# Performance work log

Measured on AMD Instinct MI355X. Metric: run time of the kernel, lower is better.

Reference implementation:

```python
import jax, jax.numpy as jnp
import numpy as np
import math

NUM_BANDS = 8
BINS = 512
CROPSIZE = 1024
BATCH = 4


def _dwconv(x, w, b):
    # depthwise Conv1d, kernel=3, padding=1, groups=C. x: [B,C,W], w: [C,1,3], b: [C]
    y = jax.lax.conv_general_dilated(x, w, window_strides=(1,), padding=((1, 1),),
                                     feature_group_count=x.shape[1])
    return y + b[None, :, None]


def setup_inputs() -> dict:
    key = jax.random.key(0)
    ks = jax.random.split(key, 20)
    s = 0.02
    lin = lambda k: jax.random.normal(k, (BINS, BINS), jnp.float32) * s
    cw = lambda k: jax.random.normal(k, (BINS, 1, 3), jnp.float32) * s
    vec = lambda k: jax.random.normal(k, (BINS,), jnp.float32) * s
    return {
        "x": jax.random.normal(ks[0], (BATCH, CROPSIZE, BINS), jnp.float32),
        "q_w": lin(ks[1]), "q_b": vec(ks[2]), "q_cw": cw(ks[3]), "q_cb": vec(ks[4]),
        "k_w": lin(ks[5]), "k_b": vec(ks[6]), "k_cw": cw(ks[7]), "k_cb": vec(ks[8]),
        "v_w": lin(ks[9]), "v_b": vec(ks[10]), "v_cw": cw(ks[11]), "v_cb": vec(ks[12]),
        "o_w": lin(ks[13]), "o_b": vec(ks[14]),
        "er": jax.random.normal(ks[15], (BINS // NUM_BANDS, CROPSIZE), jnp.float32),
    }


def reference(x, q_w, q_b, q_cw, q_cb, k_w, k_b, k_cw, k_cb,
              v_w, v_b, v_cw, v_cb, o_w, o_b, er):
    b, w, c = x.shape
    h = NUM_BANDS

    def proj(lw, lb, cwt, cbt):
        y = x @ lw.T + lb                                   # [b,w,c] linear
        y = _dwconv(y.transpose(0, 2, 1), cwt, cbt)         # [b,c,w] depthwise conv
        return y.transpose(0, 2, 1).reshape(b, w, h, -1)    # [b,w,h,d]

    q = proj(q_w, q_b, q_cw, q_cb).transpose(0, 2, 1, 3)    # [b,h,w,d]
    k = proj(k_w, k_b, k_cw, k_cb).transpose(0, 2, 3, 1)    # [b,h,d,w]
    v = proj(v_w, v_b, v_cw, v_cb).transpose(0, 2, 1, 3)    # [b,h,w,d]

    # relative position bias via pad/transpose/slice skew
    qe = jnp.einsum('bhwd,dc->bhwc', q, er)                 # [b,h,w,cropsize]
    p = jnp.pad(qe, ((0, 0), (0, 0), (0, 0), (1, 0)))       # [b,h,w,cs+1]
    p = p.transpose(0, 1, 3, 2)[:, :, 1:, :]                # [b,h,cs,w] == [b,h,w,w]

    qk = (q @ k + p) / math.sqrt(c)
    a = jax.nn.softmax(qk, axis=-1)
    out = (a @ v).transpose(0, 2, 1, 3).reshape(b, w, c)    # [b,w,c]
    return out @ o_w.T + o_b
```

## Files before the change

### kernel.cpp

```cpp
#include <hip/hip_runtime.h>
#include <hip/hip_bf16.h>
#include <math.h>


#define CROP 1024
#define NB 512
#define NH 8
#define HD 64
#define NBATCH 4
#define MTOT 4096
#define NBH 32
#define JSPLIT 4
#define ROWS_TOT 32768

typedef __attribute__((ext_vector_type(8))) short bf8;
typedef __attribute__((ext_vector_type(4))) short s4;
typedef __attribute__((ext_vector_type(4))) float f4;
typedef __attribute__((ext_vector_type(8))) _Float16 h8;

__device__ __forceinline__ short f2bf(float f) {
  __hip_bfloat16 h = __float2bfloat16(f);
  short s;
  __builtin_memcpy(&s, &h, 2);
  return s;
}
__device__ __forceinline__ float bf2f(short s) {
  union { unsigned u; float f; } v; v.u = ((unsigned)(unsigned short)s) << 16;
  return v.f;
}
__device__ __forceinline__ f4 mfma16(bf8 a, bf8 b, f4 c) {
  return __builtin_amdgcn_mfma_f32_16x16x32_bf16(a, b, c, 0, 0, 0);
}
__device__ __forceinline__ float fast_exp2(float x) {
#if __has_builtin(__builtin_amdgcn_exp2f)
  return __builtin_amdgcn_exp2f(x);
#else
  float r;
  asm("v_exp_f32 %0, %1" : "=v"(r) : "v"(x));
  return r;
#endif
}

__device__ __forceinline__ void stage16(const short* g, short* ldsbase, int lane) {
#if __has_builtin(__builtin_amdgcn_global_load_lds)
  __builtin_amdgcn_global_load_lds(
      (const __attribute__((address_space(1))) void*)g,
      (__attribute__((address_space(3))) void*)ldsbase, 16, 0, 0);
#else
  *(bf8*)(ldsbase + lane * 8) = *(const bf8*)g;
#endif
}

#define ISC 0.044194173824159216f
#define QSCALE 0.06376743237228177f

__global__ __launch_bounds__(256) void prep_kernel(
    const float* __restrict__ x,
    const float* __restrict__ w0, const float* __restrict__ w1,
    const float* __restrict__ w2, const float* __restrict__ w3,
    const float* __restrict__ er,
    short* __restrict__ xb, short* __restrict__ wb, short* __restrict__ erT)
{
  const int blk = blockIdx.x;
  const int t = threadIdx.x;
  if (blk < 1024) {
    int i = (blk * 256 + t) * 8;
    f4 a = *(const f4*)(x + i);
    f4 b = *(const f4*)(x + i + 4);
    bf8 o;
#pragma unroll
    for (int j = 0; j < 4; ++j) { o[j] = f2bf(a[j]); o[4 + j] = f2bf(b[j]); }
    *(bf8*)(xb + i) = o;
  } else if (blk < 1536) {
    int p = (blk - 1024) >> 7;
    const float* s = (p == 0) ? w0 : (p == 1) ? w1 : (p == 2) ? w2 : w3;
    int i = (((blk - 1024) & 127) * 256 + t) * 8;
    f4 a = *(const f4*)(s + i);
    f4 b = *(const f4*)(s + i + 4);
    bf8 o;
#pragma unroll
    for (int j = 0; j < 4; ++j) { o[j] = f2bf(a[j]); o[4 + j] = f2bf(b[j]); }
    *(bf8*)(wb + (size_t)p * NB * NB + i) = o;
  } else {
    int idx = (blk - 1536) * 256 + t;
    int w = idx >> 6, d = idx & 63;
    erT[idx] = f2bf(er[d * CROP + w]);
  }
}

__device__ __forceinline__ void gemm128_loop(
    const short* __restrict__ A, const short* __restrict__ Bm,
    short* As, short* Bs, int rowA0, int rowB0, f4 (&acc)[4][4], int t)
{
  const int lane = t & 63, wave = t >> 6;
  const int wr = wave >> 1, wc = wave & 1;
  const int l15 = lane & 15, l4 = lane >> 4;
  const int crow = lane >> 3;
  const int csub = lane & 7;
  const int kb = (csub * 16) ^ (crow << 4);

  for (int k0 = 0; k0 < NB; k0 += 64) {
    __syncthreads();
#pragma unroll
    for (int i = 0; i < 4; ++i) {
      const int c = wave * 4 + i;
      stage16(A + (size_t)(rowA0 + c * 8 + crow) * NB + k0 + (kb >> 1),
              As + c * 512, lane);
      stage16(Bm + (size_t)(rowB0 + c * 8 + crow) * NB + k0 + (kb >> 1),
              Bs + c * 512, lane);
    }
    __syncthreads();
#pragma unroll
    for (int ks = 0; ks < 2; ++ks) {
      bf8 af[4], bg[4];
#pragma unroll
      for (int mt = 0; mt < 4; ++mt) {
        const int row = wr * 64 + mt * 16 + l15;
        const int byt = (ks * 64 + l4 * 16) ^ ((row & 7) << 4);
        af[mt] = *(const bf8*)&As[row * 64 + (byt >> 1)];
      }
#pragma unroll
      for (int nt = 0; nt < 4; ++nt) {
        const int row = wc * 64 + nt * 16 + l15;
        const int byt = (ks * 64 + l4 * 16) ^ ((row & 7) << 4);
        bg[nt] = *(const bf8*)&Bs[row * 64 + (byt >> 1)];
      }
#pragma unroll
      for (int mt = 0; mt < 4; ++mt)
#pragma unroll
        for (int nt = 0; nt < 4; ++nt)
          acc[mt][nt] = mfma16(af[mt], bg[nt], acc[mt][nt]);
    }
  }
}

__global__ __launch_bounds__(256) void proj_gemm3(
    const short* __restrict__ Xb, const short* __restrict__ Wb,
    const float* __restrict__ B0, const float* __restrict__ B1, const float* __restrict__ B2,
    short* __restrict__ O0, short* __restrict__ O1, short* __restrict__ O2)
{
  __shared__ short As[128 * 64];
  __shared__ short Bs[128 * 64];
  f4 acc[4][4];
#pragma unroll
  for (int i = 0; i < 4; ++i)
#pragma unroll
    for (int j = 0; j < 4; ++j) acc[i][j] = (f4){0.f, 0.f, 0.f, 0.f};

  const int bm = blockIdx.x, bn = blockIdx.y;
  gemm128_loop(Xb, Wb, As, Bs, bm * 128, bn * 128, acc, threadIdx.x);

  const int p = bn >> 2;
  const float* Bb = (p == 0) ? B0 : (p == 1) ? B1 : B2;
  short* Out = (p == 0) ? O0 : (p == 1) ? O1 : O2;
  const int ncol0 = (bn & 3) * 128;

  const int t = threadIdx.x;
  const int lane = t & 63, wave = t >> 6;
  const int wr = wave >> 1, wc = wave & 1;
  const int l15 = lane & 15, l4 = lane >> 4;
#pragma unroll
  for (int mt = 0; mt < 4; ++mt)
#pragma unroll
    for (int nt = 0; nt < 4; ++nt) {
      const int col = ncol0 + wc * 64 + nt * 16 + l15;
      const float bias = Bb[col];
#pragma unroll
      for (int r = 0; r < 4; ++r) {
        const int row = bm * 128 + wr * 64 + mt * 16 + l4 * 4 + r;
        Out[(size_t)row * NB + col] = f2bf(acc[mt][nt][r] + bias);
      }
    }
}

__global__ __launch_bounds__(256) void dwconv_all(
    const short* __restrict__ q0p, const short* __restrict__ k0p,
    const short* __restrict__ v0p,
    const float* __restrict__ qcw, const float* __restrict__ qcb,
    const float* __restrict__ kcw, const float* __restrict__ kcb,
    const float* __restrict__ vcw, const float* __restrict__ vcb,
    short* __restrict__ qb, short* __restrict__ kb, short* __restrict__ vb)
{
  const int blk = blockIdx.x;
  const int t = threadIdx.x;

  if (blk < 2048) {
    const int p = blk >> 10;
    const short* src = p ? k0p : q0p;
    const float* cw = p ? kcw : qcw;
    const float* cb = p ? kcb : qcb;
    short* dst = p ? kb : qb;
    const float scale = p ? 1.0f : QSCALE;

    const int idx = ((blk & 1023) * 256 + t) * 8;
    const int c = idx & (NB - 1);
    const int m = idx >> 9;
    const int w = m & (CROP - 1);
    const int b = m >> 10;

    const bf8 z = (bf8){0, 0, 0, 0, 0, 0, 0, 0};
    bf8 mid = *(const bf8*)(src + idx);
    bf8 lo = (w > 0) ? *(const bf8*)(src + idx - NB) : z;
    bf8 hi = (w < CROP - 1) ? *(const bf8*)(src + idx + NB) : z;

    f4 cwv[6];
#pragma unroll
    for (int i = 0; i < 6; ++i) cwv[i] = *(const f4*)(cw + c * 3 + i * 4);
    f4 cb0 = *(const f4*)(cb + c);
    f4 cb1 = *(const f4*)(cb + c + 4);

    bf8 o;
#pragma unroll
    for (int j = 0; j < 8; ++j) {
      float k0w = cwv[(3 * j) >> 2][(3 * j) & 3];
      float k1w = cwv[(3 * j + 1) >> 2][(3 * j + 1) & 3];
      float k2w = cwv[(3 * j + 2) >> 2][(3 * j + 2) & 3];
      float bias = (j < 4) ? cb0[j] : cb1[j - 4];
      float acc = bias + k0w * bf2f(lo[j]) + k1w * bf2f(mid[j]) + k2w * bf2f(hi[j]);
      o[j] = f2bf(acc * scale);
    }
    const int h = c >> 6, d0 = c & 63;
    *(bf8*)(dst + ((size_t)(b * NH + h) * CROP + w) * HD + d0) = o;
  } else {
    __shared__ short S[66][72];
    const int blk2 = blk - 2048;
    const int w0 = (blk2 & 15) * 64, c0 = ((blk2 >> 4) & 7) * 64, b = blk2 >> 7;

#pragma unroll
    for (int i = 0; i < 3; ++i) {
      int r = i * 32 + (t >> 3);
      if (r < 66) {
        int w = w0 - 1 + r;
        int cg = (t & 7) * 8;
        bf8 val = (bf8){0, 0, 0, 0, 0, 0, 0, 0};
        if (w >= 0 && w < CROP)
          val = *(const bf8*)(v0p + ((size_t)b * CROP + w) * NB + c0 + cg);
        *(bf8*)&S[r][cg] = val;
      }
    }
    __syncthreads();

    const int c = t & 63, wv = t >> 6;
    const float k0w = vcw[(c0 + c) * 3 + 0];
    const float k1w = vcw[(c0 + c) * 3 + 1];
    const float k2w = vcw[(c0 + c) * 3 + 2];
    const float bias = vcb[c0 + c];

    float xa = bf2f(S[wv * 16][c]);
    float xb2 = bf2f(S[wv * 16 + 1][c]);
    short res[16];
#pragma unroll
    for (int ww = 0; ww < 16; ++ww) {
      float xc = bf2f(S[wv * 16 + ww + 2][c]);
      res[ww] = f2bf(bias + k0w * xa + k1w * xb2 + k2w * xc);
      xa = xb2; xb2 = xc;
    }
    short* dstbase = vb + ((size_t)(b * NB) + c0 + c) * CROP + w0
                     + (wv >> 1) * 32 + (wv & 1) * 4;
#pragma unroll
    for (int pidx = 0; pidx < 4; ++pidx)
      *(s4*)(dstbase + pidx * 8) = *(s4*)&res[pidx * 4];
  }
}

__global__ __launch_bounds__(512) void attn_part(
    const short* __restrict__ Qb, const short* __restrict__ Kb,
    const short* __restrict__ Vb, const short* __restrict__ ErT,
    _Float16* __restrict__ Op, float* __restrict__ lbuf)
{
  __shared__ short Ks[64][72];
  __shared__ short Qs[64][72];
  __shared__ short Vs[64][72];

  const int qt = blockIdx.x, bh = blockIdx.y, s = blockIdx.z;
  const int t = threadIdx.x;
  const int lane = t & 63, wave = t >> 6;
  const int l15 = lane & 15, l4 = lane >> 4;
  const int wq = qt * 128 + wave * 16;

  bf8 qa[2], ea[2];
  {
    const short* qrow = Qb + ((size_t)bh * CROP + wq + l15) * HD + l4 * 8;
    qa[0] = *(const bf8*)(qrow);
    qa[1] = *(const bf8*)(qrow + 32);
    const short* erow = ErT + (size_t)(wq + l15) * HD + l4 * 8;
    ea[0] = *(const bf8*)(erow);
    ea[1] = *(const bf8*)(erow + 32);
  }

  float lsum = 0.f;
  f4 oacc[4];
#pragma unroll
  for (int nt = 0; nt < 4; ++nt) oacc[nt] = (f4){0.f, 0.f, 0.f, 0.f};

  const int sr2 = t >> 3, sc2 = (t & 7) * 8;
  const short* ksrc = Kb + ((size_t)bh * CROP + sr2) * HD + sc2;
  const short* qsrc = Qb + ((size_t)bh * CROP + sr2) * HD + sc2;
  const short* vsrc = Vb + ((size_t)bh * HD + sr2) * CROP + sc2;

  const int jbase = s * (CROP / JSPLIT);
  const int JLEN = CROP / JSPLIT;

  bf8 rk = *(const bf8*)(ksrc + jbase * HD);
  bf8 rq = *(const bf8*)(qsrc + jbase * HD);
  bf8 rv = *(const bf8*)(vsrc + jbase);

  for (int jj = 0; jj < JLEN; jj += 64) {
    __syncthreads();
    *(bf8*)&Ks[sr2][sc2] = rk;
    *(bf8*)&Qs[sr2][sc2] = rq;
    *(bf8*)&Vs[sr2][sc2] = rv;
    __syncthreads();

    const int jn = jj + 64;
    if (jn < JLEN) {
      rk = *(const bf8*)(ksrc + (jbase + jn) * HD);
      rq = *(const bf8*)(qsrc + (jbase + jn) * HD);
      rv = *(const bf8*)(vsrc + jbase + jn);
    }

    f4 sacc[4];
#pragma unroll
    for (int nt = 0; nt < 4; ++nt) sacc[nt] = (f4){0.f, 0.f, 0.f, 0.f};
    __builtin_amdgcn_s_setprio(1);
#pragma unroll
    for (int ks = 0; ks < 2; ++ks) {
#pragma unroll
      for (int nt = 0; nt < 4; ++nt) {
        bf8 kf = *(bf8*)&Ks[nt * 16 + l15][ks * 32 + l4 * 8];
        sacc[nt] = mfma16(kf, qa[ks], sacc[nt]);
        bf8 qf = *(bf8*)&Qs[nt * 16 + l15][ks * 32 + l4 * 8];
        sacc[nt] = mfma16(qf, ea[ks], sacc[nt]);
      }
    }
    __builtin_amdgcn_s_setprio(0);

    bf8 pf0, pf1;
#pragma unroll
    for (int nt = 0; nt < 4; ++nt) {
      float e0 = fast_exp2(sacc[nt][0]);
      float e1 = fast_exp2(sacc[nt][1]);
      float e2 = fast_exp2(sacc[nt][2]);
      float e3 = fast_exp2(sacc[nt][3]);
      lsum += (e0 + e1) + (e2 + e3);
      if (nt < 2) {
        pf0[nt * 4 + 0] = f2bf(e0); pf0[nt * 4 + 1] = f2bf(e1);
        pf0[nt * 4 + 2] = f2bf(e2); pf0[nt * 4 + 3] = f2bf(e3);
      } else {
        pf1[(nt - 2) * 4 + 0] = f2bf(e0); pf1[(nt - 2) * 4 + 1] = f2bf(e1);
        pf1[(nt - 2) * 4 + 2] = f2bf(e2); pf1[(nt - 2) * 4 + 3] = f2bf(e3);
      }
    }

    __builtin_amdgcn_s_setprio(1);
#pragma unroll
    for (int ks = 0; ks < 2; ++ks) {
      bf8 pf = ks ? pf1 : pf0;
#pragma unroll
      for (int nt = 0; nt < 4; ++nt) {
        bf8 vf = *(bf8*)&Vs[nt * 16 + l15][ks * 32 + l4 * 8];
        oacc[nt] = mfma16(pf, vf, oacc[nt]);
      }
    }
    __builtin_amdgcn_s_setprio(0);
  }

  lsum += __shfl_xor(lsum, 16);
  lsum += __shfl_xor(lsum, 32);

#pragma unroll
  for (int r = 0; r < 4; ++r) {
    const int row = wq + l4 * 4 + r;
    const size_t ridx = (size_t)(s * NBH + bh) * CROP + row;
#pragma unroll
    for (int nt = 0; nt < 4; ++nt)
      Op[ridx * HD + nt * 16 + l15] = (_Float16)oacc[nt][r];
  }
  if (lane < 16)
    lbuf[(size_t)(s * NBH + bh) * CROP + wq + l15] = lsum;
}

__global__ __launch_bounds__(256) void attn_combine(
    const _Float16* __restrict__ Op, const float* __restrict__ lbuf,
    short* __restrict__ Ao)
{
  const int t = threadIdx.x;
  const int idx = blockIdx.x * 32 + (t >> 3);
  const int dth = (t & 7) * 8;
  float l = 0.f;
#pragma unroll
  for (int s = 0; s < JSPLIT; ++s) l += lbuf[(size_t)s * ROWS_TOT + idx];
  float inv = 1.f / l;
  float o[8] = {0, 0, 0, 0, 0, 0, 0, 0};
#pragma unroll
  for (int s = 0; s < JSPLIT; ++s) {
    h8 v = *(const h8*)(Op + ((size_t)s * ROWS_TOT + idx) * HD + dth);
#pragma unroll
    for (int j = 0; j < 8; ++j) o[j] += (float)v[j];
  }
  const int bh = idx >> 10, row = idx & (CROP - 1);
  const int b = bh >> 3, h = bh & 7;
  short* dst = Ao + ((size_t)(b * CROP + row)) * NB + h * HD + dth;
  bf8 ov;
#pragma unroll
  for (int j = 0; j < 8; ++j) ov[j] = f2bf(o[j] * inv);
  *(bf8*)dst = ov;
}

__global__ __launch_bounds__(256) void out_gemm2(
    const short* __restrict__ A, const short* __restrict__ Wt,
    const float* __restrict__ Bb, float* __restrict__ Out)
{
  __shared__ short As[64][72];
  __shared__ short Bs[64][72];
  const int t = threadIdx.x;
  const int lane = t & 63, wave = t >> 6;
  const int wr = wave >> 1, wc = wave & 1;
  const int l15 = lane & 15, l4 = lane >> 4;
  const int bm = blockIdx.x, bn = blockIdx.y;

  f4 acc[2][2];
#pragma unroll
  for (int i = 0; i < 2; ++i)
#pragma unroll
    for (int j = 0; j < 2; ++j) acc[i][j] = (f4){0.f, 0.f, 0.f, 0.f};

  const int sr = t >> 2, sc = (t & 3) * 16;
  const short* arow = A + (size_t)(bm * 64 + sr) * NB + sc;
  const short* wrow = Wt + (size_t)(bn * 64 + sr) * NB + sc;

  for (int k0 = 0; k0 < NB; k0 += 64) {
    bf8 a0 = *(const bf8*)(arow + k0);
    bf8 a1 = *(const bf8*)(arow + k0 + 8);
    bf8 b0 = *(const bf8*)(wrow + k0);
    bf8 b1 = *(const bf8*)(wrow + k0 + 8);
    __syncthreads();
    *(bf8*)&As[sr][sc] = a0;
    *(bf8*)&As[sr][sc + 8] = a1;
    *(bf8*)&Bs[sr][sc] = b0;
    *(bf8*)&Bs[sr][sc + 8] = b1;
    __syncthreads();
#pragma unroll
    for (int ks = 0; ks < 2; ++ks) {
      bf8 af[2], bg[2];
#pragma unroll
      for (int mt = 0; mt < 2; ++mt)
        af[mt] = *(bf8*)&As[wr * 32 + mt * 16 + l15][ks * 32 + l4 * 8];
#pragma unroll
      for (int nt = 0; nt < 2; ++nt)
        bg[nt] = *(bf8*)&Bs[wc * 32 + nt * 16 + l15][ks * 32 + l4 * 8];
#pragma unroll
      for (int mt = 0; mt < 2; ++mt)
#pragma unroll
        for (int nt = 0; nt < 2; ++nt)
          acc[mt][nt] = mfma16(af[mt], bg[nt], acc[mt][nt]);
    }
  }
#pragma unroll
  for (int mt = 0; mt < 2; ++mt)
#pragma unroll
    for (int nt = 0; nt < 2; ++nt)
#pragma unroll
      for (int r = 0; r < 4; ++r) {
        int row = bm * 64 + wr * 32 + mt * 16 + l4 * 4 + r;
        int col = bn * 64 + wc * 32 + nt * 16 + l15;
        Out[(size_t)row * NB + col] = acc[mt][nt][r] + Bb[col];
      }
}

extern "C" void kernel_launch(void* const* d_in, const int* in_sizes, int n_in,
                              void* d_out, int out_size, void* d_ws, size_t ws_size,
                              hipStream_t stream) {
  (void)in_sizes; (void)n_in; (void)out_size; (void)ws_size;
  const float* x    = (const float*)d_in[0];
  const float* q_w  = (const float*)d_in[1];
  const float* q_b  = (const float*)d_in[2];
  const float* q_cw = (const float*)d_in[3];
  const float* q_cb = (const float*)d_in[4];
  const float* k_w  = (const float*)d_in[5];
  const float* k_b  = (const float*)d_in[6];
  const float* k_cw = (const float*)d_in[7];
  const float* k_cb = (const float*)d_in[8];
  const float* v_w  = (const float*)d_in[9];
  const float* v_b  = (const float*)d_in[10];
  const float* v_cw = (const float*)d_in[11];
  const float* v_cb = (const float*)d_in[12];
  const float* o_w  = (const float*)d_in[13];
  const float* o_b  = (const float*)d_in[14];
  const float* er   = (const float*)d_in[15];
  float* out = (float*)d_out;

  char* ws = (char*)d_ws;
  const size_t MB = 1u << 20;
  short* q0  = (short*)(ws + 0 * MB);
  short* k0  = (short*)(ws + 4 * MB);
  short* v0  = (short*)(ws + 8 * MB);
  short* qb2 = (short*)(ws + 12 * MB);
  short* kb2 = (short*)(ws + 16 * MB);
  short* vb2 = (short*)(ws + 20 * MB);
  short* ao  = (short*)(ws + 24 * MB);
  short* erT = (short*)(ws + 28 * MB);
  short* xb  = (short*)(ws + 29 * MB);
  short* wb  = (short*)(ws + 33 * MB);
  _Float16* Op = (_Float16*)(ws + 36 * MB);
  float* lbuf  = (float*)(ws + 52 * MB);

  prep_kernel<<<dim3(1792), dim3(256), 0, stream>>>(
      x, q_w, k_w, v_w, o_w, er, xb, wb, erT);
  proj_gemm3<<<dim3(32, 12), dim3(256), 0, stream>>>(
      xb, wb, q_b, k_b, v_b, q0, k0, v0);
  dwconv_all<<<dim3(2560), dim3(256), 0, stream>>>(
      q0, k0, v0, q_cw, q_cb, k_cw, k_cb, v_cw, v_cb, qb2, kb2, vb2);
  attn_part<<<dim3(8, NBH, JSPLIT), dim3(512), 0, stream>>>(
      qb2, kb2, vb2, erT, Op, lbuf);
  attn_combine<<<dim3(1024), dim3(256), 0, stream>>>(Op, lbuf, ao);
  out_gemm2<<<dim3(64, 8), dim3(256), 0, stream>>>(
      ao, wb + 3 * NB * NB, o_b, out);
}
```

Before: 69.06 us.

## Process two query subtiles per wave in attention with 256-thread blocks

```diff
diff --git a/kernel.cpp b/kernel.cpp
--- a/kernel.cpp
+++ b/kernel.cpp
@@ -263,7 +263,7 @@
   }
 }
 
-__global__ __launch_bounds__(512) void attn_part(
+__global__ __launch_bounds__(256) void attn_part(
     const short* __restrict__ Qb, const short* __restrict__ Kb,
     const short* __restrict__ Vb, const short* __restrict__ ErT,
     _Float16* __restrict__ Op, float* __restrict__ lbuf)
@@ -276,22 +276,25 @@
   const int t = threadIdx.x;
   const int lane = t & 63, wave = t >> 6;
   const int l15 = lane & 15, l4 = lane >> 4;
-  const int wq = qt * 128 + wave * 16;
-
-  bf8 qa[2], ea[2];
-  {
-    const short* qrow = Qb + ((size_t)bh * CROP + wq + l15) * HD + l4 * 8;
-    qa[0] = *(const bf8*)(qrow);
-    qa[1] = *(const bf8*)(qrow + 32);
-    const short* erow = ErT + (size_t)(wq + l15) * HD + l4 * 8;
-    ea[0] = *(const bf8*)(erow);
-    ea[1] = *(const bf8*)(erow + 32);
-  }
-
-  float lsum = 0.f;
-  f4 oacc[4];
-#pragma unroll
-  for (int nt = 0; nt < 4; ++nt) oacc[nt] = (f4){0.f, 0.f, 0.f, 0.f};
+  const int wq = qt * 128 + wave * 32;
+
+  bf8 qa[2][2], ea[2][2];
+#pragma unroll
+  for (int ih = 0; ih < 2; ++ih) {
+    const short* qrow = Qb + ((size_t)bh * CROP + wq + ih * 16 + l15) * HD + l4 * 8;
+    qa[ih][0] = *(const bf8*)(qrow);
+    qa[ih][1] = *(const bf8*)(qrow + 32);
+    const short* erow = ErT + (size_t)(wq + ih * 16 + l15) * HD + l4 * 8;
+    ea[ih][0] = *(const bf8*)(erow);
+    ea[ih][1] = *(const bf8*)(erow + 32);
+  }
+
+  float lsum[2] = {0.f, 0.f};
+  f4 oacc[2][4];
+#pragma unroll
+  for (int ih = 0; ih < 2; ++ih)
+#pragma unroll
+    for (int nt = 0; nt < 4; ++nt) oacc[ih][nt] = (f4){0.f, 0.f, 0.f, 0.f};
 
   const int sr2 = t >> 3, sc2 = (t & 7) * 8;
   const short* ksrc = Kb + ((size_t)bh * CROP + sr2) * HD + sc2;
@@ -301,83 +304,102 @@
   const int jbase = s * (CROP / JSPLIT);
   const int JLEN = CROP / JSPLIT;
 
-  bf8 rk = *(const bf8*)(ksrc + jbase * HD);
-  bf8 rq = *(const bf8*)(qsrc + jbase * HD);
-  bf8 rv = *(const bf8*)(vsrc + jbase);
+  bf8 rk0 = *(const bf8*)(ksrc + jbase * HD);
+  bf8 rk1 = *(const bf8*)(ksrc + (jbase + 32) * HD);
+  bf8 rq0 = *(const bf8*)(qsrc + jbase * HD);
+  bf8 rq1 = *(const bf8*)(qsrc + (jbase + 32) * HD);
+  bf8 rv0 = *(const bf8*)(vsrc + jbase);
+  bf8 rv1 = *(const bf8*)(vsrc + 32 * CROP + jbase);
 
   for (int jj = 0; jj < JLEN; jj += 64) {
     __syncthreads();
-    *(bf8*)&Ks[sr2][sc2] = rk;
-    *(bf8*)&Qs[sr2][sc2] = rq;
-    *(bf8*)&Vs[sr2][sc2] = rv;
+    *(bf8*)&Ks[sr2][sc2] = rk0;
+    *(bf8*)&Ks[32 + sr2][sc2] = rk1;
+    *(bf8*)&Qs[sr2][sc2] = rq0;
+    *(bf8*)&Qs[32 + sr2][sc2] = rq1;
+    *(bf8*)&Vs[sr2][sc2] = rv0;
+    *(bf8*)&Vs[32 + sr2][sc2] = rv1;
     __syncthreads();
 
     const int jn = jj + 64;
     if (jn < JLEN) {
-      rk = *(const bf8*)(ksrc + (jbase + jn) * HD);
-      rq = *(const bf8*)(qsrc + (jbase + jn) * HD);
-      rv = *(const bf8*)(vsrc + jbase + jn);
-    }
-
-    f4 sacc[4];
-#pragma unroll
-    for (int nt = 0; nt < 4; ++nt) sacc[nt] = (f4){0.f, 0.f, 0.f, 0.f};
+      rk0 = *(const bf8*)(ksrc + (jbase + jn) * HD);
+      rk1 = *(const bf8*)(ksrc + (jbase + jn + 32) * HD);
+      rq0 = *(const bf8*)(qsrc + (jbase + jn) * HD);
+      rq1 = *(const bf8*)(qsrc + (jbase + jn + 32) * HD);
+      rv0 = *(const bf8*)(vsrc + jbase + jn);
+      rv1 = *(const bf8*)(vsrc + 32 * CROP + jbase + jn);
+    }
+
+    f4 sacc[2][4];
+#pragma unroll
+    for (int ih = 0; ih < 2; ++ih)
+#pragma unroll
+      for (int nt = 0; nt < 4; ++nt) sacc[ih][nt] = (f4){0.f, 0.f, 0.f, 0.f};
     __builtin_amdgcn_s_setprio(1);
 #pragma unroll
     for (int ks = 0; ks < 2; ++ks) {
 #pragma unroll
       for (int nt = 0; nt < 4; ++nt) {
         bf8 kf = *(bf8*)&Ks[nt * 16 + l15][ks * 32 + l4 * 8];
-        sacc[nt] = mfma16(kf, qa[ks], sacc[nt]);
+        sacc[0][nt] = mfma16(kf, qa[0][ks], sacc[0][nt]);
+        sacc[1][nt] = mfma16(kf, qa[1][ks], sacc[1][nt]);
         bf8 qf = *(bf8*)&Qs[nt * 16 + l15][ks * 32 + l4 * 8];
-        sacc[nt] = mfma16(qf, ea[ks], sacc[nt]);
+        sacc[0][nt] = mfma16(qf, ea[0][ks], sacc[0][nt]);
+        sacc[1][nt] = mfma16(qf, ea[1][ks], sacc[1][nt]);
       }
     }
     __builtin_amdgcn_s_setprio(0);
 
-    bf8 pf0, pf1;
-#pragma unroll
-    for (int nt = 0; nt < 4; ++nt) {
-      float e0 = fast_exp2(sacc[nt][0]);
-      float e1 = fast_exp2(sacc[nt][1]);
-      float e2 = fast_exp2(sacc[nt][2]);
-      float e3 = fast_exp2(sacc[nt][3]);
-      lsum += (e0 + e1) + (e2 + e3);
-      if (nt < 2) {
-        pf0[nt * 4 + 0] = f2bf(e0); pf0[nt * 4 + 1] = f2bf(e1);
-        pf0[nt * 4 + 2] = f2bf(e2); pf0[nt * 4 + 3] = f2bf(e3);
-      } else {
-        pf1[(nt - 2) * 4 + 0] = f2bf(e0); pf1[(nt - 2) * 4 + 1] = f2bf(e1);
-        pf1[(nt - 2) * 4 + 2] = f2bf(e2); pf1[(nt - 2) * 4 + 3] = f2bf(e3);
-      }
-    }
+    bf8 pf[2][2];
+#pragma unroll
+    for (int ih = 0; ih < 2; ++ih)
+#pragma unroll
+      for (int nt = 0; nt < 4; ++nt) {
+        float e0 = fast_exp2(sacc[ih][nt][0]);
+        float e1 = fast_exp2(sacc[ih][nt][1]);
+        float e2 = fast_exp2(sacc[ih][nt][2]);
+        float e3 = fast_exp2(sacc[ih][nt][3]);
+        lsum[ih] += (e0 + e1) + (e2 + e3);
+        bf8& dstp = pf[ih][nt >> 1];
+        const int base = (nt & 1) * 4;
+        dstp[base + 0] = f2bf(e0); dstp[base + 1] = f2bf(e1);
+        dstp[base + 2] = f2bf(e2); dstp[base + 3] = f2bf(e3);
+      }
 
     __builtin_amdgcn_s_setprio(1);
 #pragma unroll
     for (int ks = 0; ks < 2; ++ks) {
-      bf8 pf = ks ? pf1 : pf0;
 #pragma unroll
       for (int nt = 0; nt < 4; ++nt) {
         bf8 vf = *(bf8*)&Vs[nt * 16 + l15][ks * 32 + l4 * 8];
-        oacc[nt] = mfma16(pf, vf, oacc[nt]);
+        oacc[0][nt] = mfma16(pf[0][ks], vf, oacc[0][nt]);
+        oacc[1][nt] = mfma16(pf[1][ks], vf, oacc[1][nt]);
       }
     }
     __builtin_amdgcn_s_setprio(0);
   }
 
-  lsum += __shfl_xor(lsum, 16);
-  lsum += __shfl_xor(lsum, 32);
-
-#pragma unroll
-  for (int r = 0; r < 4; ++r) {
-    const int row = wq + l4 * 4 + r;
-    const size_t ridx = (size_t)(s * NBH + bh) * CROP + row;
-#pragma unroll
-    for (int nt = 0; nt < 4; ++nt)
-      Op[ridx * HD + nt * 16 + l15] = (_Float16)oacc[nt][r];
-  }
-  if (lane < 16)
-    lbuf[(size_t)(s * NBH + bh) * CROP + wq + l15] = lsum;
+#pragma unroll
+  for (int ih = 0; ih < 2; ++ih) {
+    lsum[ih] += __shfl_xor(lsum[ih], 16);
+    lsum[ih] += __shfl_xor(lsum[ih], 32);
+  }
+
+#pragma unroll
+  for (int ih = 0; ih < 2; ++ih)
+#pragma unroll
+    for (int r = 0; r < 4; ++r) {
+      const int row = wq + ih * 16 + l4 * 4 + r;
+      const size_t ridx = (size_t)(s * NBH + bh) * CROP + row;
+#pragma unroll
+      for (int nt = 0; nt < 4; ++nt)
+        Op[ridx * HD + nt * 16 + l15] = (_Float16)oacc[ih][nt][r];
+    }
+  if (lane < 16) {
+    lbuf[(size_t)(s * NBH + bh) * CROP + wq + l15] = lsum[0];
+    lbuf[(size_t)(s * NBH + bh) * CROP + wq + 16 + l15] = lsum[1];
+  }
 }
 
 __global__ __launch_bounds__(256) void attn_combine(
@@ -511,7 +533,7 @@
       xb, wb, q_b, k_b, v_b, q0, k0, v0);
   dwconv_all<<<dim3(2560), dim3(256), 0, stream>>>(
       q0, k0, v0, q_cw, q_cb, k_cw, k_cb, v_cw, v_cb, qb2, kb2, vb2);
-  attn_part<<<dim3(8, NBH, JSPLIT), dim3(512), 0, stream>>>(
+  attn_part<<<dim3(8, NBH, JSPLIT), dim3(256), 0, stream>>>(
       qb2, kb2, vb2, erT, Op, lbuf);
   attn_combine<<<dim3(1024), dim3(256), 0, stream>>>(Op, lbuf, ao);
   out_gemm2<<<dim3(64, 8), dim3(256), 0, stream>>>(
```

Result: no change. 69.52 us (+0.7%).
